# Kernel tuning notes

Measured on AMD Instinct MI355X. Metric: run time of the kernel, lower is better.

The kernel has to match this reference:

```python
import jax, jax.numpy as jnp
import numpy as np

OBSERVE = 30

def setup_inputs() -> dict:
    key = jax.random.key(0)
    k1, k2, k3, k4 = jax.random.split(key, 4)
    B, T = 8192, 2048
    u = jax.random.normal(k1, (B, T, 1), dtype=jnp.float32)
    x0 = jax.random.normal(k2, (B, OBSERVE), dtype=jnp.float32)
    # scale weights small so the linear AR recurrence stays stable over T steps
    W_x = jax.random.normal(k3, (OBSERVE, 1), dtype=jnp.float32) * 0.05
    W_f = jax.random.normal(k4, (1, 1), dtype=jnp.float32)
    return {"u": u, "x0": x0, "W_x": W_x, "W_f": W_f}


def reference(u, x0, W_x, W_f):
    # u: [B, T, 1]; x0: [B, observe] initial shift-register state.
    # Per step (matching the Keras cell):
    #   out = x_set @ W_x + u_t @ W_f            -> [B, 1]
    #   x_set <- concat(x_set[:, 1:], out)        (shift register)
    def step(x_set, u_t):
        out = x_set @ W_x + u_t @ W_f            # [B, 1]
        x_new = jnp.concatenate([x_set[:, 1:], out], axis=1)
        return x_new, out

    u_tbf = jnp.swapaxes(u, 0, 1)                # [T, B, 1]
    _, outs = jax.lax.scan(step, x0, u_tbf)      # outs: [T, B, 1]
    return jnp.swapaxes(outs, 0, 1)              # [B, T, 1]
```

## Files before the change

kernel.cpp:

```cpp
#include <hip/hip_runtime.h>

#define NB   8192
#define NT   2048
#define OBS  30
#define CCH  32
#define RPB  8
#define NTHR 256
#define CSTR 68

typedef float v2f __attribute__((ext_vector_type(2)));

__device__ __forceinline__ v2f step2(float (&r)[32], const v2f (&wxp)[OBS],
                                     float w29, int j, float uw0, float uw1) {
  v2f a0 = {uw0, uw1};
  v2f a1 = {0.f, 0.f};
  v2f a2 = {0.f, 0.f};
  #pragma unroll
  for (int m = 0; m < OBS; m += 3) {
    float r0 = r[(j + m) & 31], r1 = r[(j + m + 1) & 31], r2 = r[(j + m + 2) & 31];
    a0 = __builtin_elementwise_fma(wxp[m],     (v2f){r0, r0}, a0);
    a1 = __builtin_elementwise_fma(wxp[m + 1], (v2f){r1, r1}, a1);
    a2 = __builtin_elementwise_fma(wxp[m + 2], (v2f){r2, r2}, a2);
  }
  v2f A = (a0 + a1) + a2;
  float o0 = A.x;
  float o1 = fmaf(w29, o0, A.y);
  r[(j + 30) & 31] = o0;
  r[(j + 31) & 31] = o1;
  return (v2f){o0, o1};
}

__device__ __forceinline__ float dot15(const v2f (&cp)[15], const v2f (&sv)[16],
                                       float p) {
  v2f a0 = cp[0] * sv[0];
  v2f a1 = cp[1] * sv[1];
  v2f a2 = cp[2] * sv[2];
  #pragma unroll
  for (int m = 3; m < 15; m += 3) {
    a0 = __builtin_elementwise_fma(cp[m],     sv[m],     a0);
    a1 = __builtin_elementwise_fma(cp[m + 1], sv[m + 1], a1);
    a2 = __builtin_elementwise_fma(cp[m + 2], sv[m + 2], a2);
  }
  v2f A = (a0 + a1) + a2;
  return (A.x + A.y) + p;
}

__global__ void __launch_bounds__(NTHR, 2)
k_fused(const float* __restrict__ u, const float* __restrict__ x0,
        const float* __restrict__ Wx, const float* __restrict__ Wf,
        float* __restrict__ out) {
  __shared__ float tile[RPB * CCH * CSTR];
  __shared__ float Cb[64 * 33];
  __shared__ float sbuf[RPB * 32];
  const int tid  = threadIdx.x;
  const int wv   = tid >> 6;
  const int lane = tid & 63;
  const int half = lane >> 5;
  const int k    = lane & 31;
  const int row0 = blockIdx.x * RPB;
  const int lr   = wv * 2 + half;
  const int row  = row0 + lr;

  v2f wxp[OBS];
  wxp[0] = (v2f){Wx[0], 0.f};
  #pragma unroll
  for (int m = 1; m < OBS; ++m) wxp[m] = (v2f){Wx[m], Wx[m - 1]};
  const float w29 = wxp[29].x;
  const float wf  = Wf[0];
  const float x0v = (k < OBS) ? x0[(size_t)row * OBS + k] : 0.f;

  float4 stg[16];
  const float* ub = u + ((size_t)row0 + 2 * wv) * NT;
  #pragma unroll
  for (int i = 0; i < 16; ++i) {
    int v = i * 64 + lane, rr = v >> 9, p = v & 511;
    stg[i] = *(const float4*)(ub + (size_t)rr * NT + 4 * p);
  }

  if (wv == 0) {
    float r[32];
    #pragma unroll
    for (int i = 0; i < 32; ++i) r[i] = (k < OBS && i == k) ? 1.f : 0.f;
    #pragma unroll
    for (int s = 0; s < 32; ++s) {
      v2f o = step2(r, wxp, w29, (2 * s) & 31, 0.f, 0.f);
      if (lane < OBS) {
        Cb[(2 * s) * 33 + lane]     = o.x;
        Cb[(2 * s + 1) * 33 + lane] = o.y;
      }
    }
  }
  sbuf[lr * 32 + k] = x0v;

  float* sub = &tile[(wv * 2 * CCH) * CSTR];
  #pragma unroll
  for (int i = 0; i < 16; ++i) {
    int v = i * 64 + lane, rr = v >> 9, p = v & 511;
    int c = p >> 4, q = p & 15;
    *(float4*)(&sub[(rr * CCH + c) * CSTR + 4 * q]) = stg[i];
  }
  __syncthreads();

  v2f c0p[15], c1p[15];
  #pragma unroll
  for (int m = 0; m < 15; ++m)
    c0p[m] = (v2f){Cb[(2 * k) * 33 + 2 * m], Cb[(2 * k) * 33 + 2 * m + 1]};
  #pragma unroll
  for (int m = 0; m < 15; ++m)
    c1p[m] = (v2f){Cb[(2 * k + 1) * 33 + 2 * m],
                   Cb[(2 * k + 1) * 33 + 2 * m + 1]};

  {
    float r[32];
    #pragma unroll
    for (int i = 0; i < 32; ++i) r[i] = 0.f;
    float* tc = &sub[lane * CSTR];
    #pragma unroll
    for (int q = 0; q < 16; ++q) {
      float4 u4 = *(const float4*)(tc + 4 * q);
      v2f oA = step2(r, wxp, w29, (4 * q)     & 31, wf * u4.x, wf * u4.y);
      v2f oB = step2(r, wxp, w29, (4 * q + 2) & 31, wf * u4.z, wf * u4.w);
      *(float4*)(tc + 4 * q) = make_float4(oA.x, oA.y, oB.x, oB.y);
    }
  }
  __builtin_amdgcn_wave_barrier();

  float* sl = &sbuf[lr * 32];
  const float* trow = &sub[half * CCH * CSTR];
  float* orow = out + (size_t)row * NT;
  float2 pq = *(const float2*)(&trow[2 * k]);
  #pragma unroll 1
  for (int c = 0; c < CCH; ++c) {
    v2f sv2[16];
    #pragma unroll
    for (int q = 0; q < 8; ++q) {
      float4 v = *(const float4*)(sl + 4 * q);
      sv2[2 * q]     = (v2f){v.x, v.y};
      sv2[2 * q + 1] = (v2f){v.z, v.w};
    }
    int cn = (c + 1 < CCH) ? c + 1 : c;
    float2 pqn = *(const float2*)(&trow[cn * CSTR + 2 * k]);
    float t0 = dot15(c0p, sv2, pq.x);
    float t1 = dot15(c1p, sv2, pq.y);
    if (k >= 17)
      *(float2*)(&sl[2 * k - 34]) = make_float2(t0, t1);
    *(float2*)(&orow[c * 64 + 2 * k]) = make_float2(t0, t1);
    pq = pqn;
    __builtin_amdgcn_wave_barrier();
  }
}

extern "C" void kernel_launch(void* const* d_in, const int* in_sizes, int n_in,
                              void* d_out, int out_size, void* d_ws, size_t ws_size,
                              hipStream_t stream) {
  const float* u  = (const float*)d_in[0];
  const float* x0 = (const float*)d_in[1];
  const float* Wx = (const float*)d_in[2];
  const float* Wf = (const float*)d_in[3];
  float* out = (float*)d_out;

  hipLaunchKernelGGL(k_fused, dim3(NB / RPB), dim3(NTHR), 0, stream,
                     u, x0, Wx, Wf, out);
}
```

Before: 44.02 us.

## Process two row pairs per wave with prefetch of the next pair's input

```diff
diff --git a/kernel.cpp b/kernel.cpp
--- a/kernel.cpp
+++ b/kernel.cpp
@@ -4,7 +4,7 @@
 #define NT   2048
 #define OBS  30
 #define CCH  32
-#define RPB  8
+#define RPB  16
 #define NTHR 256
 #define CSTR 68
 
@@ -49,7 +49,7 @@
 k_fused(const float* __restrict__ u, const float* __restrict__ x0,
         const float* __restrict__ Wx, const float* __restrict__ Wf,
         float* __restrict__ out) {
-  __shared__ float tile[RPB * CCH * CSTR];
+  __shared__ float tile[4 * 2 * CCH * CSTR];
   __shared__ float Cb[64 * 33];
   __shared__ float sbuf[RPB * 32];
   const int tid  = threadIdx.x;
@@ -58,8 +58,7 @@
   const int half = lane >> 5;
   const int k    = lane & 31;
   const int row0 = blockIdx.x * RPB;
-  const int lr   = wv * 2 + half;
-  const int row  = row0 + lr;
+  const int wr0  = row0 + 4 * wv;
 
   v2f wxp[OBS];
   wxp[0] = (v2f){Wx[0], 0.f};
@@ -67,14 +66,17 @@
   for (int m = 1; m < OBS; ++m) wxp[m] = (v2f){Wx[m], Wx[m - 1]};
   const float w29 = wxp[29].x;
   const float wf  = Wf[0];
-  const float x0v = (k < OBS) ? x0[(size_t)row * OBS + k] : 0.f;
+  const float x0v0 = (k < OBS) ? x0[(size_t)(wr0 + half) * OBS + k] : 0.f;
+  const float x0v1 = (k < OBS) ? x0[(size_t)(wr0 + 2 + half) * OBS + k] : 0.f;
+  sbuf[(4 * wv + half) * 32 + k]     = x0v0;
+  sbuf[(4 * wv + 2 + half) * 32 + k] = x0v1;
 
   float4 stg[16];
-  const float* ub = u + ((size_t)row0 + 2 * wv) * NT;
+  const float* ubw = u + (size_t)wr0 * NT;
   #pragma unroll
   for (int i = 0; i < 16; ++i) {
     int v = i * 64 + lane, rr = v >> 9, p = v & 511;
-    stg[i] = *(const float4*)(ub + (size_t)rr * NT + 4 * p);
+    stg[i] = *(const float4*)(ubw + (size_t)rr * NT + 4 * p);
   }
 
   if (wv == 0) {
@@ -90,7 +92,6 @@
       }
     }
   }
-  sbuf[lr * 32 + k] = x0v;
 
   float* sub = &tile[(wv * 2 * CCH) * CSTR];
   #pragma unroll
@@ -110,43 +111,66 @@
     c1p[m] = (v2f){Cb[(2 * k + 1) * 33 + 2 * m],
                    Cb[(2 * k + 1) * 33 + 2 * m + 1]};
 
-  {
-    float r[32];
-    #pragma unroll
-    for (int i = 0; i < 32; ++i) r[i] = 0.f;
-    float* tc = &sub[lane * CSTR];
-    #pragma unroll
-    for (int q = 0; q < 16; ++q) {
-      float4 u4 = *(const float4*)(tc + 4 * q);
-      v2f oA = step2(r, wxp, w29, (4 * q)     & 31, wf * u4.x, wf * u4.y);
-      v2f oB = step2(r, wxp, w29, (4 * q + 2) & 31, wf * u4.z, wf * u4.w);
-      *(float4*)(tc + 4 * q) = make_float4(oA.x, oA.y, oB.x, oB.y);
+  #pragma unroll 1
+  for (int tl = 0; tl < 2; ++tl) {
+    {
+      float r[32];
+      #pragma unroll
+      for (int i = 0; i < 32; ++i) r[i] = 0.f;
+      float* tc = &sub[lane * CSTR];
+      #pragma unroll
+      for (int q = 0; q < 16; ++q) {
+        float4 u4 = *(const float4*)(tc + 4 * q);
+        v2f oA = step2(r, wxp, w29, (4 * q)     & 31, wf * u4.x, wf * u4.y);
+        v2f oB = step2(r, wxp, w29, (4 * q + 2) & 31, wf * u4.z, wf * u4.w);
+        *(float4*)(tc + 4 * q) = make_float4(oA.x, oA.y, oB.x, oB.y);
+      }
     }
-  }
-  __builtin_amdgcn_wave_barrier();
+    if (tl == 0) {
+      const float* ub1 = ubw + 2 * (size_t)NT;
+      #pragma unroll
+      for (int i = 0; i < 16; ++i) {
+        int v = i * 64 + lane, rr = v >> 9, p = v & 511;
+        stg[i] = *(const float4*)(ub1 + (size_t)rr * NT + 4 * p);
+      }
+    }
+    __builtin_amdgcn_wave_barrier();
 
-  float* sl = &sbuf[lr * 32];
-  const float* trow = &sub[half * CCH * CSTR];
-  float* orow = out + (size_t)row * NT;
-  float2 pq = *(const float2*)(&trow[2 * k]);
-  #pragma unroll 1
-  for (int c = 0; c < CCH; ++c) {
-    v2f sv2[16];
-    #pragma unroll
-    for (int q = 0; q < 8; ++q) {
-      float4 v = *(const float4*)(sl + 4 * q);
-      sv2[2 * q]     = (v2f){v.x, v.y};
-      sv2[2 * q + 1] = (v2f){v.z, v.w};
+    const int lr = 4 * wv + 2 * tl + half;
+    float* sl = &sbuf[lr * 32];
+    const float* trow = &sub[half * CCH * CSTR];
+    float* orow = out + (size_t)(row0 + lr) * NT;
+    float2 pq = *(const float2*)(&trow[2 * k]);
+    #pragma unroll 1
+    for (int c = 0; c < CCH; ++c) {
+      v2f sv2[16];
+      #pragma unroll
+      for (int q = 0; q < 8; ++q) {
+        float4 v = *(const float4*)(sl + 4 * q);
+        sv2[2 * q]     = (v2f){v.x, v.y};
+        sv2[2 * q + 1] = (v2f){v.z, v.w};
+      }
+      int cn = (c + 1 < CCH) ? c + 1 : c;
+      float2 pqn = *(const float2*)(&trow[cn * CSTR + 2 * k]);
+      float t0 = dot15(c0p, sv2, pq.x);
+      float t1 = dot15(c1p, sv2, pq.y);
+      if (k >= 17)
+        *(float2*)(&sl[2 * k - 34]) = make_float2(t0, t1);
+      *(float2*)(&orow[c * 64 + 2 * k]) = make_float2(t0, t1);
+      pq = pqn;
+      __builtin_amdgcn_wave_barrier();
     }
-    int cn = (c + 1 < CCH) ? c + 1 : c;
-    float2 pqn = *(const float2*)(&trow[cn * CSTR + 2 * k]);
-    float t0 = dot15(c0p, sv2, pq.x);
-    float t1 = dot15(c1p, sv2, pq.y);
-    if (k >= 17)
-      *(float2*)(&sl[2 * k - 34]) = make_float2(t0, t1);
-    *(float2*)(&orow[c * 64 + 2 * k]) = make_float2(t0, t1);
-    pq = pqn;
     __builtin_amdgcn_wave_barrier();
+
+    if (tl == 0) {
+      #pragma unroll
+      for (int i = 0; i < 16; ++i) {
+        int v = i * 64 + lane, rr = v >> 9, p = v & 511;
+        int c = p >> 4, q = p & 15;
+        *(float4*)(&sub[(rr * CCH + c) * CSTR + 4 * q]) = stg[i];
+      }
+      __builtin_amdgcn_wave_barrier();
+    }
   }
 }
 
```

New measurement: 57.54 us. 30.7% more time.
